# Kernel tuning notes

Hardware: AMD Instinct MI355X
Metric: run time of the kernel (lower is better)

Reference implementation:

```python
import jax, jax.numpy as jnp
import numpy as np

B, S, DIM = 2, 1024, 2048
H, NOPE, ROPE_D, VD = 16, 128, 64, 128
QKD = NOPE + ROPE_D  # 192
BASE = 10000
NEG_INF = -1e9


def _rope_cos_sin(seq_len, start_pos=0):
    # theta: [ROPE_D//2]
    theta = 1.0 / (BASE ** (jnp.arange(0, ROPE_D, 2, dtype=jnp.float32) / ROPE_D))
    pos = jnp.arange(start_pos, start_pos + seq_len, dtype=jnp.float32)
    ang = pos[:, None] * theta[None, :]  # [s, ROPE_D//2]
    return jnp.cos(ang), jnp.sin(ang)


def _apply_rope(x, cos, sin):
    # x: [b, s, h, d]; cos/sin: [s, d//2]
    b, s, h, d = x.shape
    xs = x.astype(jnp.float32).reshape(b, s, h, d // 2, 2)
    c = cos[None, :, None, :]
    sn = sin[None, :, None, :]
    out = jnp.stack([xs[..., 0] * c - xs[..., 1] * sn,
                     xs[..., 1] * c + xs[..., 0] * sn], axis=-1)
    return out.reshape(b, s, h, d).astype(x.dtype)


def setup_inputs() -> dict:
    key = jax.random.key(0)
    ks = jax.random.split(key, 6)
    x = jax.random.normal(ks[0], (B, S, DIM), dtype=jnp.float32)
    sc = lambda fan_in: 1.0 / np.sqrt(fan_in)
    Wq = jax.random.normal(ks[1], (DIM, H * QKD), dtype=jnp.float32) * sc(DIM)
    Wk = jax.random.normal(ks[2], (DIM, H * QKD), dtype=jnp.float32) * sc(DIM)
    Wv = jax.random.normal(ks[3], (DIM, H * VD), dtype=jnp.float32) * sc(DIM)
    Wo = jax.random.normal(ks[4], (H * VD, DIM), dtype=jnp.float32) * sc(H * VD)
    bo = jnp.zeros((DIM,), dtype=jnp.float32)
    mask = jnp.where(jnp.tril(jnp.ones((S, S), dtype=bool)), 0.0, NEG_INF).astype(jnp.float32)
    return {"x": x, "Wq": Wq, "Wk": Wk, "Wv": Wv, "Wo": Wo, "bo": bo,
            "mask": mask, "start_pos": 0}


def reference(x, Wq, Wk, Wv, Wo, bo, mask, start_pos):
    b, s, _ = x.shape
    q = (x @ Wq).reshape(b, s, H, QKD)
    k = (x @ Wk).reshape(b, s, H, QKD)
    v = (x @ Wv).reshape(b, s, H, VD)
    q_nope, q_rope = q[..., :NOPE], q[..., NOPE:]
    k_nope, k_rope = k[..., :NOPE], k[..., NOPE:]
    cos, sin = _rope_cos_sin(s)  # input_pos=None -> positions 0..s-1
    q_rope = _apply_rope(q_rope, cos, sin)
    k_rope = _apply_rope(k_rope, cos, sin)
    q = jnp.concatenate([q_nope, q_rope], axis=-1)
    k = jnp.concatenate([k_nope, k_rope], axis=-1)
    # start_pos=0 prefill: cache[:end_pos] == k, v just written
    scale = QKD ** -0.5
    scores = jnp.einsum('bshd,bthd->bsht', q, k) * scale
    scores = scores + mask[:, None, :]  # mask.unsqueeze(1) on [b,s,h,t] broadcasting
    weights = jax.nn.softmax(scores.astype(jnp.float32), axis=-1).astype(x.dtype)
    c_v = jnp.einsum('bsht,bthd->bshd', weights, v)
    return c_v.reshape(b, s, H * VD) @ Wo + bo
```

## Files before the change

kernel.cpp:

```cpp
#include <hip/hip_runtime.h>


typedef __bf16 bf16;
typedef __bf16 bf16x8 __attribute__((ext_vector_type(8)));
typedef __bf16 bf16x4 __attribute__((ext_vector_type(4)));
typedef float  f32x4  __attribute__((ext_vector_type(4)));

#define DEVI __device__ __forceinline__

static constexpr int Bc = 2, Sc = 1024, DIMc = 2048, Hc = 16;
static constexpr int NOPEc = 128, QKDc = 192, VDc = 128;
static constexpr int NQ    = Hc * QKDc;
static constexpr int NCAT  = NQ + NQ + Hc*VDc;

__global__ __launch_bounds__(256) void k_cvt(const float* __restrict__ in, bf16* __restrict__ out) {
    int i = (blockIdx.x * 256 + threadIdx.x) * 8;
    float4 a = *(const float4*)(in + i);
    float4 b = *(const float4*)(in + i + 4);
    bf16x8 o;
    o[0]=(bf16)a.x; o[1]=(bf16)a.y; o[2]=(bf16)a.z; o[3]=(bf16)a.w;
    o[4]=(bf16)b.x; o[5]=(bf16)b.y; o[6]=(bf16)b.z; o[7]=(bf16)b.w;
    *(bf16x8*)(out + i) = o;
}

__global__ __launch_bounds__(256) void k_transpose_all(const float* __restrict__ Wq, const float* __restrict__ Wk,
                                                       const float* __restrict__ Wv, const float* __restrict__ Wo,
                                                       bf16* __restrict__ wcat, bf16* __restrict__ woT) {
    __shared__ float tile[64][68];
    int yt = blockIdx.y;
    const float* src; bf16* dst; int N, n0;
    if (yt < 48)       { src = Wq; N = 3072; n0 = yt * 64;         dst = wcat; }
    else if (yt < 96)  { src = Wk; N = 3072; n0 = (yt - 48) * 64;  dst = wcat + (size_t)3072 * 2048; }
    else if (yt < 128) { src = Wv; N = 2048; n0 = (yt - 96) * 64;  dst = wcat + (size_t)6144 * 2048; }
    else               { src = Wo; N = 2048; n0 = (yt - 128) * 64; dst = woT; }
    int k0 = blockIdx.x * 64;
    int tr = threadIdx.x >> 4, tc = (threadIdx.x & 15) * 4;
#pragma unroll
    for (int i = 0; i < 4; i++) {
        int r = tr + i * 16;
        float4 v = *(const float4*)(src + (size_t)(k0 + r) * N + n0 + tc);
        tile[r][tc+0] = v.x; tile[r][tc+1] = v.y; tile[r][tc+2] = v.z; tile[r][tc+3] = v.w;
    }
    __syncthreads();
#pragma unroll
    for (int i = 0; i < 4; i++) {
        int n = tr + i * 16;
        bf16x4 o;
#pragma unroll
        for (int j = 0; j < 4; j++) o[j] = (bf16)tile[tc + j][n];
        *(bf16x4*)(dst + (size_t)(n0 + n) * 2048 + k0 + tc) = o;
    }
}

__global__ __launch_bounds__(256) void k_vt(const bf16* __restrict__ qkv, bf16* __restrict__ vT) {
    int st = blockIdx.x, dt = blockIdx.y, bh = blockIdx.z;
    int b = bh >> 4, h = bh & 15;
    __shared__ bf16 tile[64][72];
    int r = threadIdx.x >> 3, c8 = (threadIdx.x & 7) * 8;
    const bf16* src = qkv + (size_t)(b * Sc + st * 64) * NCAT + 2 * NQ + h * VDc + dt * 64;
#pragma unroll
    for (int i = 0; i < 2; i++) {
        int rr = r + i * 32;
        *(bf16x8*)&tile[rr][c8] = *(const bf16x8*)(src + (size_t)rr * NCAT + c8);
    }
    __syncthreads();
    bf16* dst = vT + ((size_t)bh * 128 + dt * 64) * Sc + st * 64;
#pragma unroll
    for (int i = 0; i < 2; i++) {
        int rr = r + i * 32;
        bf16x8 o;
#pragma unroll
        for (int j = 0; j < 8; j++) o[j] = tile[c8 + j][rr];
        *(bf16x8*)(dst + (size_t)rr * Sc + c8) = o;
    }
}

__global__ void k_ropetab(float* __restrict__ cosT, float* __restrict__ sinT) {
    int idx = blockIdx.x * 256 + threadIdx.x;
    int pos = idx >> 5, i = idx & 31;
    float theta = expf(-(float)i * (9.210340371976184f / 32.0f));
    float ang = (float)pos * theta;
    cosT[idx] = cosf(ang);
    sinT[idx] = sinf(ang);
}

__global__ __launch_bounds__(256) void k_rope2(bf16* __restrict__ qkv, const float* __restrict__ cosT,
                                               const float* __restrict__ sinT) {
    int bidx = blockIdx.x;
    int secbase = (bidx >= 1024) ? NQ : 0;
    int idx = (bidx & 1023) * 256 + threadIdx.x;
    int g = idx & 7, h = (idx >> 3) & 15, row = idx >> 7;
    int s = row & (Sc - 1);
    bf16* p = qkv + (size_t)row * NCAT + secbase + h * QKDc + NOPEc + g * 8;
    bf16x8 v = *(bf16x8*)p;
    const float* cp = cosT + s * 32 + g * 4;
    const float* sp = sinT + s * 32 + g * 4;
#pragma unroll
    for (int q = 0; q < 4; q++) {
        float x0 = (float)v[2*q], x1 = (float)v[2*q+1];
        float c = cp[q], sn = sp[q];
        v[2*q]   = (bf16)(x0 * c - x1 * sn);
        v[2*q+1] = (bf16)(x1 * c + x0 * sn);
    }
    *(bf16x8*)p = v;
}

DEVI void gload16(const bf16* g, bf16* l) {
    __builtin_amdgcn_global_load_lds((const __attribute__((address_space(1))) void*)g,
                                     (__attribute__((address_space(3))) void*)l, 16, 0, 0);
}

__global__ __launch_bounds__(512, 2) void k_gemm8(const bf16* __restrict__ A, const bf16* __restrict__ Bt,
                                                  bf16* __restrict__ C, int N, int K, int NCT) {
    __shared__ __align__(16) bf16 lds[2][2][2][256 * 32];
    const int tid = threadIdx.x;
    const int l = tid & 63, wid = tid >> 6;
    const int lg = l >> 4, lc = l & 15;
    const int wm = wid >> 2, wn = wid & 3;
    const int bid = blockIdx.x;
    const int xcd = bid & 7, g = bid >> 3;
    const int per = NCT >> 3;
    const int rt = g & 7, ct = xcd * per + (g >> 3);
    const int row0 = rt * 256, col0 = ct * 256;
    const int NT = K >> 6;

    const bf16* Abase = A  + (size_t)row0 * K;
    const bf16* Bbase = Bt + (size_t)col0 * K;

    size_t srcoff0, srcoff1;
    int ldsoff0, ldsoff1;
    {
        int li0 = tid,        r0 = li0 >> 2, u0 = li0 & 3;
        int li1 = 512 + tid,  r1 = li1 >> 2, u1 = li1 & 3;
        srcoff0 = (size_t)r0 * K + ((u0 ^ ((r0 >> 1) & 3)) << 3);  ldsoff0 = li0 * 8;
        srcoff1 = (size_t)r1 * K + ((u1 ^ ((r1 >> 1) & 3)) << 3);  ldsoff1 = li1 * 8;
    }

#define STAGE8(ab, ks, ktile, buf) { \
    const bf16* gb_ = ((ab) ? Bbase : Abase) + (ktile) * 64 + (ks) * 32; \
    bf16* lb_ = &lds[buf][ab][ks][0]; \
    gload16(gb_ + srcoff0, lb_ + ldsoff0); \
    gload16(gb_ + srcoff1, lb_ + ldsoff1); }

    f32x4 acc[8][4] = {};

    STAGE8(0, 0, 0, 0); STAGE8(1, 0, 0, 0); STAGE8(0, 1, 0, 0); STAGE8(1, 1, 0, 0);
    asm volatile("s_waitcnt vmcnt(4)" ::: "memory");
    __builtin_amdgcn_s_barrier();
    asm volatile("" ::: "memory");

    for (int kt = 0; kt < NT; ++kt) {
        const int cur = kt & 1, nxt = cur ^ 1;
        const bool notlast = (kt + 1 < NT);
        bf16x8 aF[4], bB[4];
#pragma unroll
        for (int ph = 0; ph < 4; ph++) {
            const int ks = ph >> 1, mh = ph & 1;
            const bf16* As_ = &lds[cur][0][ks][0];
            const bf16* Bs_ = &lds[cur][1][ks][0];
            if (mh == 0) {
#pragma unroll
                for (int fc = 0; fc < 4; fc++) {
                    int row = wn * 64 + fc * 16 + lc;
                    bB[fc] = *(const bf16x8*)(Bs_ + row * 32 + ((lg ^ ((row >> 1) & 3)) << 3));
                }
            }
#pragma unroll
            for (int i = 0; i < 4; i++) {
                int row = wm * 128 + (mh * 4 + i) * 16 + lc;
                aF[i] = *(const bf16x8*)(As_ + row * 32 + ((lg ^ ((row >> 1) & 3)) << 3));
            }
            if (notlast) {
                if      (ph == 0) STAGE8(0, 0, kt + 1, nxt)
                else if (ph == 1) STAGE8(1, 0, kt + 1, nxt)
                else if (ph == 2) STAGE8(0, 1, kt + 1, nxt)
                else              STAGE8(1, 1, kt + 1, nxt)
            }
            __builtin_amdgcn_s_barrier();
            asm volatile("" ::: "memory");
            __builtin_amdgcn_s_setprio(1);
#pragma unroll
            for (int i = 0; i < 4; i++)
#pragma unroll
                for (int fc = 0; fc < 4; fc++)
                    acc[mh * 4 + i][fc] =
                        __builtin_amdgcn_mfma_f32_16x16x32_bf16(aF[i], bB[fc], acc[mh * 4 + i][fc], 0, 0, 0);
            __builtin_amdgcn_s_setprio(0);
            if (ph == 1) {
                if (notlast) asm volatile("s_waitcnt vmcnt(4)" ::: "memory");
                else         asm volatile("s_waitcnt vmcnt(0)" ::: "memory");
            }
            if (ph == 3 && notlast) {
                asm volatile("s_waitcnt vmcnt(4)" ::: "memory");
            }
            __builtin_amdgcn_s_barrier();
            asm volatile("" ::: "memory");
        }
    }
#undef STAGE8
#pragma unroll
    for (int m = 0; m < 8; m++)
#pragma unroll
        for (int fc = 0; fc < 4; fc++)
#pragma unroll
            for (int j = 0; j < 4; j++) {
                int r = row0 + wm * 128 + m * 16 + lg * 4 + j;
                int c = col0 + wn * 64 + fc * 16 + lc;
                C[(size_t)r * N + c] = (bf16)acc[m][fc][j];
            }
}

__global__ __launch_bounds__(512, 2) void k_gemmO(const bf16* __restrict__ A, const bf16* __restrict__ Bt,
                                                  float* __restrict__ C, const float* __restrict__ bias,
                                                  int N, int K) {
    __shared__ __align__(16) bf16 lds[2][2][2][128 * 32];
    const int tid = threadIdx.x;
    const int l = tid & 63, wid = tid >> 6;
    const int lg = l >> 4, lc = l & 15;
    const int wm = wid >> 2, wn = wid & 3;
    const int bid = blockIdx.x;
    const int xcd = bid & 7, g = bid >> 3;
    const int rt = g & 15, ct = xcd * 2 + (g >> 4);
    const int row0 = rt * 128, col0 = ct * 128;
    const int NT = K >> 6;

    const bf16* Abase = A  + (size_t)row0 * K;
    const bf16* Bbase = Bt + (size_t)col0 * K;

    size_t srcoff; int ldsoff;
    {
        int r0 = tid >> 2, u0 = tid & 3;
        srcoff = (size_t)r0 * K + ((u0 ^ ((r0 >> 1) & 3)) << 3);
        ldsoff = tid * 8;
    }

#define STAGEO(ab, ks, ktile, buf) { \
    const bf16* gb_ = ((ab) ? Bbase : Abase) + (ktile) * 64 + (ks) * 32; \
    gload16(gb_ + srcoff, &lds[buf][ab][ks][0] + ldsoff); }

    f32x4 acc[4][2] = {};

    STAGEO(0, 0, 0, 0); STAGEO(1, 0, 0, 0); STAGEO(0, 1, 0, 0); STAGEO(1, 1, 0, 0);
    asm volatile("s_waitcnt vmcnt(2)" ::: "memory");
    __builtin_amdgcn_s_barrier();
    asm volatile("" ::: "memory");

    for (int kt = 0; kt < NT; ++kt) {
        const int cur = kt & 1, nxt = cur ^ 1;
        const bool notlast = (kt + 1 < NT);
#pragma unroll
        for (int ph = 0; ph < 2; ph++) {
            const bf16* As_ = &lds[cur][0][ph][0];
            const bf16* Bs_ = &lds[cur][1][ph][0];
            bf16x8 aF[4], bB[2];
#pragma unroll
            for (int n = 0; n < 2; n++) {
                int row = wn * 32 + n * 16 + lc;
                bB[n] = *(const bf16x8*)(Bs_ + row * 32 + ((lg ^ ((row >> 1) & 3)) << 3));
            }
#pragma unroll
            for (int m = 0; m < 4; m++) {
                int row = wm * 64 + m * 16 + lc;
                aF[m] = *(const bf16x8*)(As_ + row * 32 + ((lg ^ ((row >> 1) & 3)) << 3));
            }
            if (notlast) {
                if (ph == 0) { STAGEO(0, 0, kt + 1, nxt); STAGEO(1, 0, kt + 1, nxt); }
                else         { STAGEO(0, 1, kt + 1, nxt); STAGEO(1, 1, kt + 1, nxt); }
            }
            __builtin_amdgcn_s_barrier();
            asm volatile("" ::: "memory");
            __builtin_amdgcn_s_setprio(1);
#pragma unroll
            for (int m = 0; m < 4; m++)
#pragma unroll
                for (int n = 0; n < 2; n++)
                    acc[m][n] = __builtin_amdgcn_mfma_f32_16x16x32_bf16(aF[m], bB[n], acc[m][n], 0, 0, 0);
            __builtin_amdgcn_s_setprio(0);
            if (notlast)          asm volatile("s_waitcnt vmcnt(2)" ::: "memory");
            else if (ph == 0)     asm volatile("s_waitcnt vmcnt(0)" ::: "memory");
            __builtin_amdgcn_s_barrier();
            asm volatile("" ::: "memory");
        }
    }
#undef STAGEO
#pragma unroll
    for (int m = 0; m < 4; m++)
#pragma unroll
        for (int n = 0; n < 2; n++)
#pragma unroll
            for (int j = 0; j < 4; j++) {
                int r = row0 + wm * 64 + m * 16 + lg * 4 + j;
                int c = col0 + wn * 32 + n * 16 + lc;
                C[(size_t)r * N + c] = acc[m][n][j] + bias[c];
            }
}

__global__ __launch_bounds__(256, 3) void k_attn(const bf16* __restrict__ qkv, const bf16* __restrict__ vT,
                                                 bf16* __restrict__ cv) {
    const int bid = blockIdx.x;
    const int xcd = bid & 7, g = bid >> 3;
    const int qt = 15 - (g & 15);
    const int bh = xcd + 8 * (g >> 4);
    const int b = bh >> 4, h = bh & 15;
    const int tid = threadIdx.x, l = tid & 63, w = tid >> 6;
    const int lg = l >> 4, lc = l & 15;
    __shared__ __align__(16) bf16 Ks[64 * 192];
    __shared__ __align__(16) bf16 Vs[128 * 64];
    __shared__ __align__(16) bf16 Pl[4][16][72];
    const bf16* Qb = qkv + (size_t)b * Sc * NCAT + h * QKDc;
    const bf16* Kb = Qb + NQ;
    const bf16* Vt = vT + (size_t)bh * 128 * Sc;

    int sK[6];
#pragma unroll
    for (int r = 0; r < 6; r++) {
        int li = r * 256 + tid;
        int row = li / 24, c16 = li - row * 24;
        sK[r] = row * NCAT + ((c16 ^ (row & 7)) * 8);
    }
    int sV[4];
#pragma unroll
    for (int r = 0; r < 4; r++) {
        int li = r * 256 + tid;
        int row = li >> 3, c16 = li & 7;
        sV[r] = row * Sc + ((c16 ^ (row & 7)) * 8);
    }
    const int swz = lc & 7;

    bf16x8 qF[6];
    const int qrow = qt * 64 + w * 16 + lc;
#pragma unroll
    for (int kc = 0; kc < 6; kc++) qF[kc] = *(const bf16x8*)(Qb + (size_t)qrow * NCAT + kc * 32 + lg * 8);

    f32x4 acc[8] = {};
    float mrow[4] = {-1e30f, -1e30f, -1e30f, -1e30f};
    float lsum[4] = {0.f, 0.f, 0.f, 0.f};
    const float scale = 0.07216878364870323f;

#pragma unroll
    for (int r = 0; r < 6; r++) gload16(Kb + sK[r], Ks + (r * 256 + tid) * 8);

    for (int c = 0; c <= qt; ++c) {
        const int t0 = c * 64;
        __syncthreads();
#pragma unroll
        for (int r = 0; r < 4; r++) gload16(Vt + t0 + sV[r], Vs + (r * 256 + tid) * 8);
        f32x4 sc[4] = {};
#pragma unroll
        for (int nt = 0; nt < 4; nt++)
#pragma unroll
            for (int kc = 0; kc < 6; kc++) {
                bf16x8 kf = *(const bf16x8*)(Ks + (nt * 16 + lc) * 192 + (((kc * 4 + lg) ^ swz) * 8));
                sc[nt] = __builtin_amdgcn_mfma_f32_16x16x32_bf16(qF[kc], kf, sc[nt], 0, 0, 0);
            }
        __syncthreads();
        if (c < qt) {
#pragma unroll
            for (int r = 0; r < 6; r++) gload16(Kb + (size_t)(t0 + 64) * NCAT + sK[r], Ks + (r * 256 + tid) * 8);
        }
        float p[4][4];
        float cmax[4] = {-1e30f, -1e30f, -1e30f, -1e30f};
        const bool diag = (c == qt);
#pragma unroll
        for (int nt = 0; nt < 4; nt++)
#pragma unroll
            for (int j = 0; j < 4; j++) {
                float v = sc[nt][j] * scale;
                if (diag) {
                    int tg = t0 + nt * 16 + lc;
                    int rg = qt * 64 + w * 16 + lg * 4 + j;
                    if (tg > rg) v = -1e9f;
                }
                p[nt][j] = v;
                cmax[j] = fmaxf(cmax[j], v);
            }
#pragma unroll
        for (int j = 0; j < 4; j++)
#pragma unroll
            for (int d = 1; d < 16; d <<= 1) cmax[j] = fmaxf(cmax[j], __shfl_xor(cmax[j], d));
        float f[4];
#pragma unroll
        for (int j = 0; j < 4; j++) {
            float nm = fmaxf(mrow[j], cmax[j]);
            f[j] = __expf(mrow[j] - nm);
            mrow[j] = nm;
        }
        float psum[4] = {0.f, 0.f, 0.f, 0.f};
#pragma unroll
        for (int nt = 0; nt < 4; nt++)
#pragma unroll
            for (int j = 0; j < 4; j++) {
                p[nt][j] = __expf(p[nt][j] - mrow[j]);
                psum[j] += p[nt][j];
            }
#pragma unroll
        for (int j = 0; j < 4; j++) {
#pragma unroll
            for (int d = 1; d < 16; d <<= 1) psum[j] += __shfl_xor(psum[j], d);
            lsum[j] = lsum[j] * f[j] + psum[j];
        }
#pragma unroll
        for (int n = 0; n < 8; n++)
#pragma unroll
            for (int j = 0; j < 4; j++) acc[n][j] *= f[j];
#pragma unroll
        for (int nt = 0; nt < 4; nt++)
#pragma unroll
            for (int j = 0; j < 4; j++)
                Pl[w][lg * 4 + j][nt * 16 + lc] = (bf16)p[nt][j];
#pragma unroll
        for (int ks = 0; ks < 2; ks++) {
            bf16x8 aP = *(const bf16x8*)(&Pl[w][lc][ks * 32 + lg * 8]);
#pragma unroll
            for (int n = 0; n < 8; n++) {
                bf16x8 bV = *(const bf16x8*)(Vs + (n * 16 + lc) * 64 + (((ks * 4 + lg) ^ swz) * 8));
                acc[n] = __builtin_amdgcn_mfma_f32_16x16x32_bf16(aP, bV, acc[n], 0, 0, 0);
            }
        }
    }
#pragma unroll
    for (int j = 0; j < 4; j++) {
        float inv = 1.0f / lsum[j];
        int r = qt * 64 + w * 16 + lg * 4 + j;
#pragma unroll
        for (int n = 0; n < 8; n++) {
            float v = acc[n][j] * inv;
            cv[((size_t)(b * Sc + r) * Hc + h) * VDc + n * 16 + lc] = (bf16)v;
        }
    }
}

extern "C" void kernel_launch(void* const* d_in, const int* in_sizes, int n_in,
                              void* d_out, int out_size, void* d_ws, size_t ws_size,
                              hipStream_t stream) {
    const float* x  = (const float*)d_in[0];
    const float* Wq = (const float*)d_in[1];
    const float* Wk = (const float*)d_in[2];
    const float* Wv = (const float*)d_in[3];
    const float* Wo = (const float*)d_in[4];
    const float* bo = (const float*)d_in[5];
    float* out = (float*)d_out;
    char* ws = (char*)d_ws;

    bf16*  wcat = (bf16*)(ws + 0);
    bf16*  woT  = (bf16*)(ws + 33554432);
    bf16*  xb   = (bf16*)(ws + 41943040);
    bf16*  qkvb = (bf16*)(ws + 50331648);
    bf16*  cvb  = (bf16*)(ws + 83886080);
    bf16*  vTb  = (bf16*)(ws + 92274688);
    float* cosT = (float*)(ws + 100663296);
    float* sinT = (float*)(ws + 100794368);

    k_cvt<<<2048, 256, 0, stream>>>(x, xb);
    k_transpose_all<<<dim3(32, 160), 256, 0, stream>>>(Wq, Wk, Wv, Wo, wcat, woT);
    k_ropetab<<<128, 256, 0, stream>>>(cosT, sinT);
    k_gemm8<<<256, 512, 0, stream>>>(xb, wcat, qkvb, NCAT, DIMc, NCAT / 256);
    k_rope2<<<2048, 256, 0, stream>>>(qkvb, cosT, sinT);
    k_vt<<<dim3(16, 2, 32), 256, 0, stream>>>(qkvb, vTb);
    k_attn<<<512, 256, 0, stream>>>(qkvb, vTb, cvb);
    k_gemmO<<<256, 512, 0, stream>>>(cvb, woT, out, bo, DIMc, DIMc);
}
```

Before: 177.0 us.

## Fuse RoPE into QKV GEMM epilogue and merge prep kernels into one launch

Applies rotary embedding inside the QKV GEMM epilogue, using lane shuffles to pair adjacent columns, so the separate read-modify-write rope pass disappears. The input conversion, weight transposes and rope-table generation are merged into one kernel to cut launch count. The GEMM main loop is also restructured from four phases to two, loading all eight A fragments per phase with fewer barriers. This raises register pressure and makes the epilogue gather cos/sin values.

```diff
diff --git a/kernel.cpp b/kernel.cpp
--- a/kernel.cpp
+++ b/kernel.cpp
@@ -13,42 +13,55 @@
 static constexpr int NQ    = Hc * QKDc;
 static constexpr int NCAT  = NQ + NQ + Hc*VDc;
 
-__global__ __launch_bounds__(256) void k_cvt(const float* __restrict__ in, bf16* __restrict__ out) {
-    int i = (blockIdx.x * 256 + threadIdx.x) * 8;
-    float4 a = *(const float4*)(in + i);
-    float4 b = *(const float4*)(in + i + 4);
-    bf16x8 o;
-    o[0]=(bf16)a.x; o[1]=(bf16)a.y; o[2]=(bf16)a.z; o[3]=(bf16)a.w;
-    o[4]=(bf16)b.x; o[5]=(bf16)b.y; o[6]=(bf16)b.z; o[7]=(bf16)b.w;
-    *(bf16x8*)(out + i) = o;
-}
-
-__global__ __launch_bounds__(256) void k_transpose_all(const float* __restrict__ Wq, const float* __restrict__ Wk,
-                                                       const float* __restrict__ Wv, const float* __restrict__ Wo,
-                                                       bf16* __restrict__ wcat, bf16* __restrict__ woT) {
+__global__ __launch_bounds__(256) void k_prep(const float* __restrict__ x,
+                                              const float* __restrict__ Wq, const float* __restrict__ Wk,
+                                              const float* __restrict__ Wv, const float* __restrict__ Wo,
+                                              bf16* __restrict__ xb, bf16* __restrict__ wcat,
+                                              bf16* __restrict__ woT,
+                                              float* __restrict__ cosT, float* __restrict__ sinT) {
     __shared__ float tile[64][68];
-    int yt = blockIdx.y;
-    const float* src; bf16* dst; int N, n0;
-    if (yt < 48)       { src = Wq; N = 3072; n0 = yt * 64;         dst = wcat; }
-    else if (yt < 96)  { src = Wk; N = 3072; n0 = (yt - 48) * 64;  dst = wcat + (size_t)3072 * 2048; }
-    else if (yt < 128) { src = Wv; N = 2048; n0 = (yt - 96) * 64;  dst = wcat + (size_t)6144 * 2048; }
-    else               { src = Wo; N = 2048; n0 = (yt - 128) * 64; dst = woT; }
-    int k0 = blockIdx.x * 64;
-    int tr = threadIdx.x >> 4, tc = (threadIdx.x & 15) * 4;
-#pragma unroll
-    for (int i = 0; i < 4; i++) {
-        int r = tr + i * 16;
-        float4 v = *(const float4*)(src + (size_t)(k0 + r) * N + n0 + tc);
-        tile[r][tc+0] = v.x; tile[r][tc+1] = v.y; tile[r][tc+2] = v.z; tile[r][tc+3] = v.w;
-    }
-    __syncthreads();
-#pragma unroll
-    for (int i = 0; i < 4; i++) {
-        int n = tr + i * 16;
-        bf16x4 o;
-#pragma unroll
-        for (int j = 0; j < 4; j++) o[j] = (bf16)tile[tc + j][n];
-        *(bf16x4*)(dst + (size_t)(n0 + n) * 2048 + k0 + tc) = o;
+    const int yt = blockIdx.y, xt = blockIdx.x, tid = threadIdx.x;
+    if (yt < 160) {
+        const float* src; bf16* dst; int N, n0;
+        if (yt < 48)       { src = Wq; N = 3072; n0 = yt * 64;         dst = wcat; }
+        else if (yt < 96)  { src = Wk; N = 3072; n0 = (yt - 48) * 64;  dst = wcat + (size_t)3072 * 2048; }
+        else if (yt < 128) { src = Wv; N = 2048; n0 = (yt - 96) * 64;  dst = wcat + (size_t)6144 * 2048; }
+        else               { src = Wo; N = 2048; n0 = (yt - 128) * 64; dst = woT; }
+        int k0 = xt * 64;
+        int tr = tid >> 4, tc = (tid & 15) * 4;
+#pragma unroll
+        for (int i = 0; i < 4; i++) {
+            int r = tr + i * 16;
+            float4 v = *(const float4*)(src + (size_t)(k0 + r) * N + n0 + tc);
+            tile[r][tc+0] = v.x; tile[r][tc+1] = v.y; tile[r][tc+2] = v.z; tile[r][tc+3] = v.w;
+        }
+        __syncthreads();
+#pragma unroll
+        for (int i = 0; i < 4; i++) {
+            int n = tr + i * 16;
+            bf16x4 o;
+#pragma unroll
+            for (int j = 0; j < 4; j++) o[j] = (bf16)tile[tc + j][n];
+            *(bf16x4*)(dst + (size_t)(n0 + n) * 2048 + k0 + tc) = o;
+        }
+    } else if (yt < 224) {
+        int i = (((yt - 160) * 32 + xt) * 256 + tid) * 8;
+        float4 a = *(const float4*)(x + i);
+        float4 b = *(const float4*)(x + i + 4);
+        bf16x8 o;
+        o[0]=(bf16)a.x; o[1]=(bf16)a.y; o[2]=(bf16)a.z; o[3]=(bf16)a.w;
+        o[4]=(bf16)b.x; o[5]=(bf16)b.y; o[6]=(bf16)b.z; o[7]=(bf16)b.w;
+        *(bf16x8*)(xb + i) = o;
+    } else {
+#pragma unroll
+        for (int p = 0; p < 4; p++) {
+            int idx = p * 8192 + xt * 256 + tid;
+            int pos = idx >> 5, i = idx & 31;
+            float theta = expf(-(float)i * (9.210340371976184f / 32.0f));
+            float ang = (float)pos * theta;
+            cosT[idx] = cosf(ang);
+            sinT[idx] = sinf(ang);
+        }
     }
 }
 
@@ -75,43 +88,14 @@
     }
 }
 
-__global__ void k_ropetab(float* __restrict__ cosT, float* __restrict__ sinT) {
-    int idx = blockIdx.x * 256 + threadIdx.x;
-    int pos = idx >> 5, i = idx & 31;
-    float theta = expf(-(float)i * (9.210340371976184f / 32.0f));
-    float ang = (float)pos * theta;
-    cosT[idx] = cosf(ang);
-    sinT[idx] = sinf(ang);
-}
-
-__global__ __launch_bounds__(256) void k_rope2(bf16* __restrict__ qkv, const float* __restrict__ cosT,
-                                               const float* __restrict__ sinT) {
-    int bidx = blockIdx.x;
-    int secbase = (bidx >= 1024) ? NQ : 0;
-    int idx = (bidx & 1023) * 256 + threadIdx.x;
-    int g = idx & 7, h = (idx >> 3) & 15, row = idx >> 7;
-    int s = row & (Sc - 1);
-    bf16* p = qkv + (size_t)row * NCAT + secbase + h * QKDc + NOPEc + g * 8;
-    bf16x8 v = *(bf16x8*)p;
-    const float* cp = cosT + s * 32 + g * 4;
-    const float* sp = sinT + s * 32 + g * 4;
-#pragma unroll
-    for (int q = 0; q < 4; q++) {
-        float x0 = (float)v[2*q], x1 = (float)v[2*q+1];
-        float c = cp[q], sn = sp[q];
-        v[2*q]   = (bf16)(x0 * c - x1 * sn);
-        v[2*q+1] = (bf16)(x1 * c + x0 * sn);
-    }
-    *(bf16x8*)p = v;
-}
-
 DEVI void gload16(const bf16* g, bf16* l) {
     __builtin_amdgcn_global_load_lds((const __attribute__((address_space(1))) void*)g,
                                      (__attribute__((address_space(3))) void*)l, 16, 0, 0);
 }
 
 __global__ __launch_bounds__(512, 2) void k_gemm8(const bf16* __restrict__ A, const bf16* __restrict__ Bt,
-                                                  bf16* __restrict__ C, int N, int K, int NCT) {
+                                                  bf16* __restrict__ C, int N, int K, int NCT,
+                                                  const float* __restrict__ cosT, const float* __restrict__ sinT) {
     __shared__ __align__(16) bf16 lds[2][2][2][256 * 32];
     const int tid = threadIdx.x;
     const int l = tid & 63, wid = tid >> 6;
@@ -152,45 +136,38 @@
     for (int kt = 0; kt < NT; ++kt) {
         const int cur = kt & 1, nxt = cur ^ 1;
         const bool notlast = (kt + 1 < NT);
-        bf16x8 aF[4], bB[4];
-#pragma unroll
-        for (int ph = 0; ph < 4; ph++) {
-            const int ks = ph >> 1, mh = ph & 1;
-            const bf16* As_ = &lds[cur][0][ks][0];
-            const bf16* Bs_ = &lds[cur][1][ks][0];
-            if (mh == 0) {
-#pragma unroll
-                for (int fc = 0; fc < 4; fc++) {
-                    int row = wn * 64 + fc * 16 + lc;
-                    bB[fc] = *(const bf16x8*)(Bs_ + row * 32 + ((lg ^ ((row >> 1) & 3)) << 3));
-                }
-            }
-#pragma unroll
-            for (int i = 0; i < 4; i++) {
-                int row = wm * 128 + (mh * 4 + i) * 16 + lc;
+#pragma unroll
+        for (int ph = 0; ph < 2; ph++) {
+            const bf16* As_ = &lds[cur][0][ph][0];
+            const bf16* Bs_ = &lds[cur][1][ph][0];
+            bf16x8 aF[8], bB[4];
+#pragma unroll
+            for (int fc = 0; fc < 4; fc++) {
+                int row = wn * 64 + fc * 16 + lc;
+                bB[fc] = *(const bf16x8*)(Bs_ + row * 32 + ((lg ^ ((row >> 1) & 3)) << 3));
+            }
+#pragma unroll
+            for (int i = 0; i < 8; i++) {
+                int row = wm * 128 + i * 16 + lc;
                 aF[i] = *(const bf16x8*)(As_ + row * 32 + ((lg ^ ((row >> 1) & 3)) << 3));
             }
             if (notlast) {
-                if      (ph == 0) STAGE8(0, 0, kt + 1, nxt)
-                else if (ph == 1) STAGE8(1, 0, kt + 1, nxt)
-                else if (ph == 2) STAGE8(0, 1, kt + 1, nxt)
-                else              STAGE8(1, 1, kt + 1, nxt)
+                if (ph == 0) { STAGE8(0, 0, kt + 1, nxt); STAGE8(1, 0, kt + 1, nxt); }
+                else         { STAGE8(0, 1, kt + 1, nxt); STAGE8(1, 1, kt + 1, nxt); }
             }
             __builtin_amdgcn_s_barrier();
             asm volatile("" ::: "memory");
             __builtin_amdgcn_s_setprio(1);
 #pragma unroll
-            for (int i = 0; i < 4; i++)
+            for (int i = 0; i < 8; i++)
 #pragma unroll
                 for (int fc = 0; fc < 4; fc++)
-                    acc[mh * 4 + i][fc] =
-                        __builtin_amdgcn_mfma_f32_16x16x32_bf16(aF[i], bB[fc], acc[mh * 4 + i][fc], 0, 0, 0);
+                    acc[i][fc] = __builtin_amdgcn_mfma_f32_16x16x32_bf16(aF[i], bB[fc], acc[i][fc], 0, 0, 0);
             __builtin_amdgcn_s_setprio(0);
-            if (ph == 1) {
+            if (ph == 0) {
                 if (notlast) asm volatile("s_waitcnt vmcnt(4)" ::: "memory");
                 else         asm volatile("s_waitcnt vmcnt(0)" ::: "memory");
-            }
-            if (ph == 3 && notlast) {
+            } else if (notlast) {
                 asm volatile("s_waitcnt vmcnt(4)" ::: "memory");
             }
             __builtin_amdgcn_s_barrier();
@@ -201,13 +178,23 @@
 #pragma unroll
     for (int m = 0; m < 8; m++)
 #pragma unroll
-        for (int fc = 0; fc < 4; fc++)
+        for (int fc = 0; fc < 4; fc++) {
+            const int c0 = col0 + wn * 64 + fc * 16;
+            const bool ropeg = (c0 < 2 * NQ) && ((c0 % QKDc) >= NOPEc);
+            const int ip = ((c0 % QKDc) - NOPEc + lc) >> 1;
 #pragma unroll
             for (int j = 0; j < 4; j++) {
                 int r = row0 + wm * 128 + m * 16 + lg * 4 + j;
-                int c = col0 + wn * 64 + fc * 16 + lc;
-                C[(size_t)r * N + c] = (bf16)acc[m][fc][j];
-            }
+                float v = acc[m][fc][j];
+                if (ropeg) {
+                    int s = r & (Sc - 1);
+                    float cv = cosT[s * 32 + ip], sv = sinT[s * 32 + ip];
+                    float pr = __shfl_xor(v, 1);
+                    v = (lc & 1) ? (v * cv + pr * sv) : (v * cv - pr * sv);
+                }
+                C[(size_t)r * N + c0 + lc] = (bf16)v;
+            }
+        }
 }
 
 __global__ __launch_bounds__(512, 2) void k_gemmO(const bf16* __restrict__ A, const bf16* __restrict__ Bt,
@@ -451,11 +438,8 @@
     float* cosT = (float*)(ws + 100663296);
     float* sinT = (float*)(ws + 100794368);
 
-    k_cvt<<<2048, 256, 0, stream>>>(x, xb);
-    k_transpose_all<<<dim3(32, 160), 256, 0, stream>>>(Wq, Wk, Wv, Wo, wcat, woT);
-    k_ropetab<<<128, 256, 0, stream>>>(cosT, sinT);
-    k_gemm8<<<256, 512, 0, stream>>>(xb, wcat, qkvb, NCAT, DIMc, NCAT / 256);
-    k_rope2<<<2048, 256, 0, stream>>>(qkvb, cosT, sinT);
+    k_prep<<<dim3(32, 225), 256, 0, stream>>>(x, Wq, Wk, Wv, Wo, xb, wcat, woT, cosT, sinT);
+    k_gemm8<<<256, 512, 0, stream>>>(xb, wcat, qkvb, NCAT, DIMc, NCAT / 256, cosT, sinT);
     k_vt<<<dim3(16, 2, 32), 256, 0, stream>>>(qkvb, vTb);
     k_attn<<<512, 256, 0, stream>>>(qkvb, vTb, cvb);
     k_gemmO<<<256, 512, 0, stream>>>(cvb, woT, out, bo, DIMc, DIMc);
```

Result: slower. 186.4 us (+5.3%).
